# Optimization experiments

Measured on AMD Instinct MI355X. Metric: run time of the kernel, lower is better.

Reference implementation:

```python
import jax, jax.numpy as jnp
import numpy as np

N = 50000      # cells (nodes)
E = 1600000    # directed edges (kNN connectivity graph)
F_IN = 2000    # highly-variable genes
HID = 16
H = 4          # GAT heads
C = 16         # GAT out channels per head
NUM_CLASSES = 3


def setup_inputs() -> dict:
    key = jax.random.key(0)
    ks = jax.random.split(key, 10)
    x = jax.random.normal(ks[0], (N, F_IN), dtype=jnp.float32)
    edge_index = jax.random.randint(ks[1], (2, E), 0, N, dtype=jnp.int64)
    s = 0.05
    W1 = jax.random.normal(ks[2], (F_IN, HID), dtype=jnp.float32) * s
    b1 = jnp.zeros((HID,), jnp.float32)
    Wg = jax.random.normal(ks[3], (HID, H * C), dtype=jnp.float32) * s
    att_src = jax.random.normal(ks[4], (H, C), dtype=jnp.float32) * s
    att_dst = jax.random.normal(ks[5], (H, C), dtype=jnp.float32) * s
    bg = jnp.zeros((H * C,), jnp.float32)
    Wo = jax.random.normal(ks[6], (H * C, NUM_CLASSES), dtype=jnp.float32) * s
    bo = jnp.zeros((NUM_CLASSES,), jnp.float32)
    return {"x": x, "edge_index": edge_index, "W1": W1, "b1": b1, "Wg": Wg,
            "att_src": att_src, "att_dst": att_dst, "bg": bg, "Wo": Wo, "bo": bo}


def reference(x, edge_index, W1, b1, Wg, att_src, att_dst, bg, Wo, bo):
    n = x.shape[0]
    loops = jnp.arange(n, dtype=edge_index.dtype)
    src = jnp.concatenate([edge_index[0], loops])  # [E+N]
    dst = jnp.concatenate([edge_index[1], loops])

    # ---- GCNConv(F_IN -> 16): project, symmetric-normalize, scatter-add ----
    h = x @ W1                                                   # [N, 16]
    deg = jax.ops.segment_sum(jnp.ones(src.shape, h.dtype), dst, num_segments=n)
    dinv = jnp.where(deg > 0, jax.lax.rsqrt(deg), 0.0)
    norm = dinv[src] * dinv[dst]                                 # [E+N]
    h = jax.ops.segment_sum(h[src] * norm[:, None], dst, num_segments=n) + b1
    h = jax.nn.relu(h)                                           # dropout is identity in eval

    # ---- GATConv(16 -> 16, heads=4, concat) ----
    g = (h @ Wg).reshape(n, H, C)                                # [N, H, C]
    a_s = jnp.einsum('nhc,hc->nh', g, att_src)                   # [N, H]
    a_d = jnp.einsum('nhc,hc->nh', g, att_dst)
    e = jax.nn.leaky_relu(a_s[src] + a_d[dst], 0.2)              # [E+N, H]
    m = jax.ops.segment_max(e, dst, num_segments=n)              # segment softmax (stable)
    ex = jnp.exp(e - m[dst])
    denom = jax.ops.segment_sum(ex, dst, num_segments=n)
    alpha = ex / (denom[dst] + 1e-16)                            # [E+N, H]
    out = jax.ops.segment_sum(g[src] * alpha[:, :, None], dst, num_segments=n)
    out = out.reshape(n, H * C) + bg                             # [N, 64]

    # ---- classifier head ----
    logits = out @ Wo + bo                                       # [N, 3]
    return jax.nn.log_softmax(logits, axis=1)
```

## Files before the change

### kernel.cpp

```cpp
#include <hip/hip_runtime.h>
#include <hip/hip_bf16.h>
#include <math.h>

#define F_IN   2000
#define HID    16
#define HEADS  4
#define CPH    16
#define HC     64
#define NCLS   3

__device__ __forceinline__ float lrelu(float x){ return x > 0.f ? x : 0.2f*x; }

__device__ __forceinline__ float comp4(const float4& v, int k){
  return k==0 ? v.x : k==1 ? v.y : k==2 ? v.z : v.w;
}

__device__ __forceinline__ float bf2f(unsigned short u){
  return __uint_as_float(((unsigned)u) << 16);
}

__global__ void k_zero(int* __restrict__ deg, int n) {
  int i = blockIdx.x * 256 + threadIdx.x;
  if (i < n) deg[i] = 0;
}

__global__ __launch_bounds__(256) void k_gemm_deg(const float* __restrict__ x,
                                                  const float* __restrict__ W1,
                                                  __hip_bfloat16* __restrict__ h0b,
                                                  int n, int ngemm,
                                                  const int* __restrict__ edst,
                                                  int* __restrict__ deg, int e) {
  __shared__ float w1s[8192];
  if ((int)blockIdx.x >= ngemm) {
    int i = (blockIdx.x - ngemm) * 256 + threadIdx.x;
    if (i < e) atomicAdd(&deg[edst[i]], 1);
    return;
  }
  const int t    = threadIdx.x;
  const int lane = t & 63;
  const int wid  = t >> 6;
  const int rowbase = blockIdx.x * 16 + wid * 4;

  float acc[64];
  #pragma unroll
  for (int v = 0; v < 64; ++v) acc[v] = 0.f;

  for (int phase = 0; phase < 4; ++phase) {
    const int kbase = phase * 500;
    __syncthreads();
    #pragma unroll
    for (int k = 0; k < 8; ++k) {
      const int slotbase = (wid * 8 + k) * 64;
      const int slot = slotbase + lane;
      const int row_slot = slot >> 2;
      const int r = row_slot ^ ((row_slot >> 4) & 1);
      const int q = (slot & 3) ^ ((row_slot >> 2) & 3);
      int rg = kbase + r;
      if (rg > 1999) rg = 1999;
      __builtin_amdgcn_global_load_lds(
          (const __attribute__((address_space(1))) void*)(W1 + (size_t)rg * 16 + q * 4),
          (__attribute__((address_space(3))) void*)(w1s + (size_t)slotbase * 4),
          16, 0, 0);
    }
    __syncthreads();

    #pragma unroll
    for (int i = 0; i < 2; ++i) {
      int f4l = i * 64 + lane;
      if (f4l < 125) {
        float4 xv[4];
        #pragma unroll
        for (int r = 0; r < 4; ++r) {
          int row = rowbase + r;
          xv[r] = (row < n)
              ? *reinterpret_cast<const float4*>(
                    x + (size_t)row * F_IN + kbase + f4l * 4)
              : make_float4(0.f, 0.f, 0.f, 0.f);
        }
        const int qx = f4l & 3;
        const int xb = (f4l >> 2) & 1;
        #pragma unroll
        for (int kk = 0; kk < 4; ++kk) {
          const int rs = (4 * f4l + kk) ^ xb;
          const float* rowp = w1s + rs * 16;
          float xk0 = comp4(xv[0], kk), xk1 = comp4(xv[1], kk);
          float xk2 = comp4(xv[2], kk), xk3 = comp4(xv[3], kk);
          #pragma unroll
          for (int q = 0; q < 4; ++q) {
            float4 w4 = *reinterpret_cast<const float4*>(rowp + ((q ^ qx) << 2));
            acc[0*16+4*q+0] += xk0 * w4.x; acc[0*16+4*q+1] += xk0 * w4.y;
            acc[0*16+4*q+2] += xk0 * w4.z; acc[0*16+4*q+3] += xk0 * w4.w;
            acc[1*16+4*q+0] += xk1 * w4.x; acc[1*16+4*q+1] += xk1 * w4.y;
            acc[1*16+4*q+2] += xk1 * w4.z; acc[1*16+4*q+3] += xk1 * w4.w;
            acc[2*16+4*q+0] += xk2 * w4.x; acc[2*16+4*q+1] += xk2 * w4.y;
            acc[2*16+4*q+2] += xk2 * w4.z; acc[2*16+4*q+3] += xk2 * w4.w;
            acc[3*16+4*q+0] += xk3 * w4.x; acc[3*16+4*q+1] += xk3 * w4.y;
            acc[3*16+4*q+2] += xk3 * w4.z; acc[3*16+4*q+3] += xk3 * w4.w;
          }
        }
      }
    }
  }

  #pragma unroll
  for (int b = 32; b >= 1; b >>= 1) {
    bool hi = (lane & b) != 0;
    #pragma unroll
    for (int j = 0; j < b; ++j) {
      float send = hi ? acc[j] : acc[b + j];
      float recv = __shfl_xor(send, b);
      acc[j] = (hi ? acc[b + j] : acc[j]) + recv;
    }
  }
  int r = lane >> 4, c = lane & 15;
  int row = rowbase + r;
  if (row < n) h0b[(size_t)row * 16 + c] = __float2bfloat16(acc[0]);
}

__global__ void k_scan_a(const int* __restrict__ deg, int* __restrict__ bsum, int n) {
  __shared__ int s[256];
  int i = blockIdx.x * 256 + threadIdx.x;
  s[threadIdx.x] = (i < n) ? deg[i] : 0;
  __syncthreads();
  for (int off = 128; off > 0; off >>= 1) {
    if (threadIdx.x < off) s[threadIdx.x] += s[threadIdx.x + off];
    __syncthreads();
  }
  if (threadIdx.x == 0) bsum[blockIdx.x] = s[0];
}

__global__ void k_scan_b(int* __restrict__ bsum, int nb) {
  int lane = threadIdx.x;
  int carry = 0;
  for (int base = 0; base < nb; base += 64) {
    int idx = base + lane;
    int orig = (idx < nb) ? bsum[idx] : 0;
    int v = orig;
    #pragma unroll
    for (int off = 1; off < 64; off <<= 1) {
      int tv = __shfl_up(v, off);
      if (lane >= off) v += tv;
    }
    if (idx < nb) bsum[idx] = carry + v - orig;
    carry += __shfl(v, 63);
  }
}

__global__ void k_scan_c(const int* __restrict__ deg, const int* __restrict__ bsum,
                         int* __restrict__ rowptr, int* __restrict__ cursor,
                         float* __restrict__ dinv, int n) {
  __shared__ int s[256];
  int i = blockIdx.x * 256 + threadIdx.x;
  int v = (i < n) ? deg[i] : 0;
  s[threadIdx.x] = v;
  __syncthreads();
  for (int off = 1; off < 256; off <<= 1) {
    int tv = (threadIdx.x >= off) ? s[threadIdx.x - off] : 0;
    __syncthreads();
    s[threadIdx.x] += tv;
    __syncthreads();
  }
  int excl = s[threadIdx.x] - v + bsum[blockIdx.x];
  if (i < n) {
    rowptr[i] = excl;
    cursor[i] = excl;
    dinv[i] = rsqrtf((float)(v + 1));
    if (i == n - 1) rowptr[n] = excl + v;
  }
}

__global__ void k_scatter(const int* __restrict__ esrc, const int* __restrict__ edst,
                          int* __restrict__ cursor, int* __restrict__ csr, int e) {
  int i = blockIdx.x * 256 + threadIdx.x;
  if (i < e) {
    int d = edst[i];
    int pos = atomicAdd(&cursor[d], 1);
    csr[pos] = esrc[i];
  }
}

__global__ __launch_bounds__(256) void k_gcn(
    const unsigned short* __restrict__ h0b, const int* __restrict__ rowptr,
    const int* __restrict__ csr, const float* __restrict__ dinv,
    const float* __restrict__ b1, const float* __restrict__ Wg,
    const float* __restrict__ atts, const float* __restrict__ attd,
    __hip_bfloat16* __restrict__ gb, float* __restrict__ a_s,
    float* __restrict__ a_d, int n) {
  __shared__ float wgs[HID * HC];
  __shared__ float ats[HC], atd[HC];
  int t = threadIdx.x;
  for (int i = t; i < HID * HC; i += 256) wgs[i] = Wg[i];
  if (t < HC) { ats[t] = atts[t]; atd[t] = attd[t]; }
  __syncthreads();

  int lane = t & 63, w = t >> 6;
  int dst = blockIdx.x * 4 + w;
  if (dst >= n) return;
  int j = lane >> 4, c = lane & 15;
  int start = rowptr[dst], end = rowptr[dst + 1];
  float dd = dinv[dst];

  float acc = 0.f;
  for (int idx = start + j; idx < end; idx += 4) {
    int src = csr[idx];
    acc += bf2f(h0b[(size_t)src * 16 + c]) * dinv[src];
  }
  acc += __shfl_xor(acc, 16);
  acc += __shfl_xor(acc, 32);
  acc = acc * dd + bf2f(h0b[(size_t)dst * 16 + c]) * dd * dd;
  float hv = fmaxf(acc + b1[c], 0.f);

  float go = 0.f;
  #pragma unroll
  for (int k = 0; k < 16; ++k) {
    float hk = __shfl(hv, k);
    go += hk * wgs[k * HC + lane];
  }
  gb[(size_t)dst * HC + lane] = __float2bfloat16(go);

  float asv = go * ats[lane], adv = go * atd[lane];
  #pragma unroll
  for (int m = 1; m < 16; m <<= 1) {
    asv += __shfl_xor(asv, m);
    adv += __shfl_xor(adv, m);
  }
  if (c == 0) {
    a_s[(size_t)dst * 4 + j] = asv;
    a_d[(size_t)dst * 4 + j] = adv;
  }
}

__global__ __launch_bounds__(256) void k_gat(
    const unsigned short* __restrict__ gb, const int* __restrict__ rowptr,
    const int* __restrict__ csr, const float* __restrict__ a_s,
    const float* __restrict__ a_d, const float* __restrict__ bg,
    const float* __restrict__ Wo, const float* __restrict__ bo,
    float* __restrict__ out, int n) {
  __shared__ float wos[HC * NCLS];
  __shared__ float bgs[HC];
  __shared__ float bos[NCLS];
  int t = threadIdx.x;
  if (t < HC * NCLS) wos[t] = Wo[t];
  if (t < HC) bgs[t] = bg[t];
  if (t < NCLS) bos[t] = bo[t];
  __syncthreads();

  int lane = t & 63, w = t >> 6;
  int dst = blockIdx.x * 4 + w;
  if (dst >= n) return;
  int start = rowptr[dst], end = rowptr[dst + 1];
  int j = lane >> 4, c = lane & 15, h = c >> 2;

  float adh = a_d[(size_t)dst * 4 + h];
  float ash = a_s[(size_t)dst * 4 + h];

  float m = -1e30f, den = 0.f;
  float a0 = 0.f, a1 = 0.f, a2 = 0.f, a3 = 0.f;

  for (int idx = start + j; idx < end; idx += 4) {
    int src = csr[idx];
    float e = lrelu(a_s[(size_t)src * 4 + h] + adh);
    float mn = fmaxf(m, e);
    float corr = __expf(m - mn);
    float p = __expf(e - mn);
    ushort4 u4 = *reinterpret_cast<const ushort4*>(gb + (size_t)src * HC + c * 4);
    den = den * corr + p;
    a0 = a0 * corr + p * bf2f(u4.x);
    a1 = a1 * corr + p * bf2f(u4.y);
    a2 = a2 * corr + p * bf2f(u4.z);
    a3 = a3 * corr + p * bf2f(u4.w);
    m = mn;
  }
  if (j == 0) {
    float e = lrelu(ash + adh);
    float mn = fmaxf(m, e);
    float corr = __expf(m - mn);
    float p = __expf(e - mn);
    ushort4 u4 = *reinterpret_cast<const ushort4*>(gb + (size_t)dst * HC + c * 4);
    den = den * corr + p;
    a0 = a0 * corr + p * bf2f(u4.x);
    a1 = a1 * corr + p * bf2f(u4.y);
    a2 = a2 * corr + p * bf2f(u4.z);
    a3 = a3 * corr + p * bf2f(u4.w);
    m = mn;
  }

  #pragma unroll
  for (int msk = 16; msk <= 32; msk <<= 1) {
    float m2 = __shfl_xor(m, msk);
    float d2 = __shfl_xor(den, msk);
    float b0 = __shfl_xor(a0, msk);
    float b1v = __shfl_xor(a1, msk);
    float b2 = __shfl_xor(a2, msk);
    float b3 = __shfl_xor(a3, msk);
    float M = fmaxf(m, m2);
    float c1 = __expf(m - M), c2 = __expf(m2 - M);
    den = den * c1 + d2 * c2;
    a0 = a0 * c1 + b0 * c2;
    a1 = a1 * c1 + b1v * c2;
    a2 = a2 * c1 + b2 * c2;
    a3 = a3 * c1 + b3 * c2;
    m = M;
  }
  den += 1e-16f;

  float o0 = a0 / den + bgs[c * 4 + 0];
  float o1 = a1 / den + bgs[c * 4 + 1];
  float o2 = a2 / den + bgs[c * 4 + 2];
  float o3 = a3 / den + bgs[c * 4 + 3];

  float p0 = 0.f, p1 = 0.f, p2 = 0.f;
  {
    int ch = c * 4;
    p0 += o0 * wos[(ch+0)*NCLS+0] + o1 * wos[(ch+1)*NCLS+0] + o2 * wos[(ch+2)*NCLS+0] + o3 * wos[(ch+3)*NCLS+0];
    p1 += o0 * wos[(ch+0)*NCLS+1] + o1 * wos[(ch+1)*NCLS+1] + o2 * wos[(ch+2)*NCLS+1] + o3 * wos[(ch+3)*NCLS+1];
    p2 += o0 * wos[(ch+0)*NCLS+2] + o1 * wos[(ch+1)*NCLS+2] + o2 * wos[(ch+2)*NCLS+2] + o3 * wos[(ch+3)*NCLS+2];
  }
  #pragma unroll
  for (int msk = 1; msk < 16; msk <<= 1) {
    p0 += __shfl_xor(p0, msk);
    p1 += __shfl_xor(p1, msk);
    p2 += __shfl_xor(p2, msk);
  }
  p0 += bos[0]; p1 += bos[1]; p2 += bos[2];
  float mx = fmaxf(p0, fmaxf(p1, p2));
  float ls = mx + logf(__expf(p0 - mx) + __expf(p1 - mx) + __expf(p2 - mx));
  if (lane == 0) {
    out[(size_t)dst * 3 + 0] = p0 - ls;
    out[(size_t)dst * 3 + 1] = p1 - ls;
    out[(size_t)dst * 3 + 2] = p2 - ls;
  }
}

extern "C" void kernel_launch(void* const* d_in, const int* in_sizes, int n_in,
                              void* d_out, int out_size, void* d_ws, size_t ws_size,
                              hipStream_t stream) {
  const float* x    = (const float*)d_in[0];
  const int*   ei   = (const int*)  d_in[1];
  const float* W1   = (const float*)d_in[2];
  const float* b1   = (const float*)d_in[3];
  const float* Wg   = (const float*)d_in[4];
  const float* atts = (const float*)d_in[5];
  const float* attd = (const float*)d_in[6];
  const float* bg   = (const float*)d_in[7];
  const float* Wo   = (const float*)d_in[8];
  const float* bo   = (const float*)d_in[9];
  float* out = (float*)d_out;

  const int n = in_sizes[0] / F_IN;
  const int e = in_sizes[1] / 2;
  const int* esrc = ei;
  const int* edst = ei + e;

  char* p = (char*)d_ws;
  auto alloc = [&](size_t bytes) { char* r = p; p += (bytes + 255) & ~(size_t)255; return r; };
  __hip_bfloat16* h0b = (__hip_bfloat16*)alloc((size_t)n * 16 * 2);
  int*   deg    = (int*)  alloc((size_t)n * 4);
  int*   cursor = (int*)  alloc((size_t)n * 4);
  float* dinv   = (float*)alloc((size_t)n * 4);
  int*   rowptr = (int*)  alloc((size_t)(n + 1) * 4);
  int*   bsum   = (int*)  alloc(4096);
  int*   csr    = (int*)  alloc((size_t)e * 4);
  __hip_bfloat16* gbuf = (__hip_bfloat16*)alloc((size_t)n * HC * 2);
  float* as_    = (float*)alloc((size_t)n * 4 * 4);
  float* ad_    = (float*)alloc((size_t)n * 4 * 4);

  int nzb = (n + 255) / 256;
  k_zero<<<nzb, 256, 0, stream>>>(deg, n);

  const int ngemm = (n + 15) / 16;
  const int ndeg  = (e + 255) / 256;
  k_gemm_deg<<<ngemm + ndeg, 256, 0, stream>>>(x, W1, h0b, n, ngemm, edst, deg, e);

  int nb = (n + 255) / 256;
  k_scan_a<<<nb, 256, 0, stream>>>(deg, bsum, n);
  k_scan_b<<<1, 64, 0, stream>>>(bsum, nb);
  k_scan_c<<<nb, 256, 0, stream>>>(deg, bsum, rowptr, cursor, dinv, n);

  k_scatter<<<(e + 255) / 256, 256, 0, stream>>>(esrc, edst, cursor, csr, e);

  k_gcn<<<(n + 3) / 4, 256, 0, stream>>>((const unsigned short*)h0b, rowptr, csr,
                                         dinv, b1, Wg, atts, attd,
                                         gbuf, as_, ad_, n);

  k_gat<<<(n + 3) / 4, 256, 0, stream>>>((const unsigned short*)gbuf, rowptr, csr,
                                         as_, ad_, bg, Wo, bo, out, n);
}
```

Baseline: 437.2 us.

## Give each wave a private W1 LDS tile and drop block barriers in GEMM

The x@W1 GEMM moves from 256-thread blocks sharing one W1 tile to 128-thread blocks in which every wave stages its own 256-row W1 tile in LDS. Staging now goes through registers instead of global_load_lds, so the __syncthreads around staging are gone. The K loop is re-phased to 8 chunks of 256 so every lane does useful work each phase. The aim is to remove barrier stalls and idle lanes; the cost is that W1 is re-read from cache once per 4 output rows, which greatly raises cache traffic, plus an extra register round-trip for staging.

```diff
diff --git a/kernel.cpp b/kernel.cpp
--- a/kernel.cpp
+++ b/kernel.cpp
@@ -24,7 +24,7 @@
   if (i < n) deg[i] = 0;
 }
 
-__global__ __launch_bounds__(256) void k_gemm_deg(const float* __restrict__ x,
+__global__ __launch_bounds__(128) void k_gemm_deg(const float* __restrict__ x,
                                                   const float* __restrict__ W1,
                                                   __hip_bfloat16* __restrict__ h0b,
                                                   int n, int ngemm,
@@ -32,71 +32,74 @@
                                                   int* __restrict__ deg, int e) {
   __shared__ float w1s[8192];
   if ((int)blockIdx.x >= ngemm) {
-    int i = (blockIdx.x - ngemm) * 256 + threadIdx.x;
+    int i = (blockIdx.x - ngemm) * 128 + threadIdx.x;
     if (i < e) atomicAdd(&deg[edst[i]], 1);
     return;
   }
   const int t    = threadIdx.x;
   const int lane = t & 63;
   const int wid  = t >> 6;
-  const int rowbase = blockIdx.x * 16 + wid * 4;
+  const int rowbase = blockIdx.x * 8 + wid * 4;
+  float* __restrict__ myw = w1s + wid * 4096;
 
   float acc[64];
   #pragma unroll
   for (int v = 0; v < 64; ++v) acc[v] = 0.f;
 
-  for (int phase = 0; phase < 4; ++phase) {
-    const int kbase = phase * 500;
-    __syncthreads();
+  for (int phase = 0; phase < 8; ++phase) {
+    const int kbase = phase * 256;
+    const int nrows = (kbase + 256 <= 2000) ? 256 : (2000 - kbase);
     #pragma unroll
-    for (int k = 0; k < 8; ++k) {
-      const int slotbase = (wid * 8 + k) * 64;
-      const int slot = slotbase + lane;
-      const int row_slot = slot >> 2;
-      const int r = row_slot ^ ((row_slot >> 4) & 1);
-      const int q = (slot & 3) ^ ((row_slot >> 2) & 3);
-      int rg = kbase + r;
-      if (rg > 1999) rg = 1999;
-      __builtin_amdgcn_global_load_lds(
-          (const __attribute__((address_space(1))) void*)(W1 + (size_t)rg * 16 + q * 4),
-          (__attribute__((address_space(3))) void*)(w1s + (size_t)slotbase * 4),
-          16, 0, 0);
-    }
-    __syncthreads();
-
+    for (int rnd = 0; rnd < 2; ++rnd) {
+      float4 sreg[8];
+      #pragma unroll
+      for (int b = 0; b < 8; ++b) {
+        const int slot = rnd * 512 + b * 64 + lane;
+        const int row_slot = slot >> 2;
+        const int r = row_slot ^ ((row_slot >> 4) & 1);
+        const int q = (slot & 3) ^ ((row_slot >> 2) & 3);
+        int rg = kbase + r;
+        if (rg > 1999) rg = 1999;
+        sreg[b] = *reinterpret_cast<const float4*>(W1 + (size_t)rg * 16 + q * 4);
+      }
+      #pragma unroll
+      for (int b = 0; b < 8; ++b) {
+        const int slot = rnd * 512 + b * 64 + lane;
+        *reinterpret_cast<float4*>(myw + (size_t)slot * 4) = sreg[b];
+      }
+    }
+    const int f4l = lane;
+    const int flim = nrows >> 2;
+    const bool valid = (f4l < flim);
+    float4 xv[4];
     #pragma unroll
-    for (int i = 0; i < 2; ++i) {
-      int f4l = i * 64 + lane;
-      if (f4l < 125) {
-        float4 xv[4];
+    for (int r = 0; r < 4; ++r) {
+      int row = rowbase + r;
+      xv[r] = (valid && row < n)
+          ? *reinterpret_cast<const float4*>(
+                x + (size_t)row * F_IN + kbase + f4l * 4)
+          : make_float4(0.f, 0.f, 0.f, 0.f);
+    }
+    if (valid) {
+      const int qx = f4l & 3;
+      const int xb = (f4l >> 2) & 1;
+      #pragma unroll
+      for (int kk = 0; kk < 4; ++kk) {
+        const int rs = (4 * f4l + kk) ^ xb;
+        const float* rowp = myw + rs * 16;
+        float xk0 = comp4(xv[0], kk), xk1 = comp4(xv[1], kk);
+        float xk2 = comp4(xv[2], kk), xk3 = comp4(xv[3], kk);
         #pragma unroll
-        for (int r = 0; r < 4; ++r) {
-          int row = rowbase + r;
-          xv[r] = (row < n)
-              ? *reinterpret_cast<const float4*>(
-                    x + (size_t)row * F_IN + kbase + f4l * 4)
-              : make_float4(0.f, 0.f, 0.f, 0.f);
-        }
-        const int qx = f4l & 3;
-        const int xb = (f4l >> 2) & 1;
-        #pragma unroll
-        for (int kk = 0; kk < 4; ++kk) {
-          const int rs = (4 * f4l + kk) ^ xb;
-          const float* rowp = w1s + rs * 16;
-          float xk0 = comp4(xv[0], kk), xk1 = comp4(xv[1], kk);
-          float xk2 = comp4(xv[2], kk), xk3 = comp4(xv[3], kk);
-          #pragma unroll
-          for (int q = 0; q < 4; ++q) {
-            float4 w4 = *reinterpret_cast<const float4*>(rowp + ((q ^ qx) << 2));
-            acc[0*16+4*q+0] += xk0 * w4.x; acc[0*16+4*q+1] += xk0 * w4.y;
-            acc[0*16+4*q+2] += xk0 * w4.z; acc[0*16+4*q+3] += xk0 * w4.w;
-            acc[1*16+4*q+0] += xk1 * w4.x; acc[1*16+4*q+1] += xk1 * w4.y;
-            acc[1*16+4*q+2] += xk1 * w4.z; acc[1*16+4*q+3] += xk1 * w4.w;
-            acc[2*16+4*q+0] += xk2 * w4.x; acc[2*16+4*q+1] += xk2 * w4.y;
-            acc[2*16+4*q+2] += xk2 * w4.z; acc[2*16+4*q+3] += xk2 * w4.w;
-            acc[3*16+4*q+0] += xk3 * w4.x; acc[3*16+4*q+1] += xk3 * w4.y;
-            acc[3*16+4*q+2] += xk3 * w4.z; acc[3*16+4*q+3] += xk3 * w4.w;
-          }
+        for (int q = 0; q < 4; ++q) {
+          float4 w4 = *reinterpret_cast<const float4*>(rowp + ((q ^ qx) << 2));
+          acc[0*16+4*q+0] += xk0 * w4.x; acc[0*16+4*q+1] += xk0 * w4.y;
+          acc[0*16+4*q+2] += xk0 * w4.z; acc[0*16+4*q+3] += xk0 * w4.w;
+          acc[1*16+4*q+0] += xk1 * w4.x; acc[1*16+4*q+1] += xk1 * w4.y;
+          acc[1*16+4*q+2] += xk1 * w4.z; acc[1*16+4*q+3] += xk1 * w4.w;
+          acc[2*16+4*q+0] += xk2 * w4.x; acc[2*16+4*q+1] += xk2 * w4.y;
+          acc[2*16+4*q+2] += xk2 * w4.z; acc[2*16+4*q+3] += xk2 * w4.w;
+          acc[3*16+4*q+0] += xk3 * w4.x; acc[3*16+4*q+1] += xk3 * w4.y;
+          acc[3*16+4*q+2] += xk3 * w4.z; acc[3*16+4*q+3] += xk3 * w4.w;
         }
       }
     }
@@ -368,9 +371,9 @@
   int nzb = (n + 255) / 256;
   k_zero<<<nzb, 256, 0, stream>>>(deg, n);
 
-  const int ngemm = (n + 15) / 16;
-  const int ndeg  = (e + 255) / 256;
-  k_gemm_deg<<<ngemm + ndeg, 256, 0, stream>>>(x, W1, h0b, n, ngemm, edst, deg, e);
+  const int ngemm = (n + 7) / 8;
+  const int ndeg  = (e + 127) / 128;
+  k_gemm_deg<<<ngemm + ndeg, 128, 0, stream>>>(x, W1, h0b, n, ngemm, edst, deg, e);
 
   int nb = (n + 255) / 256;
   k_scan_a<<<nb, 256, 0, stream>>>(deg, bsum, n);
```

Measured after the change: 662.0 us. 1.51x slower.
